# Optimization experiments

Measured on AMD Instinct MI355X. Metric: run time of the kernel, lower is better.

## Reference

```python
import jax, jax.numpy as jnp
import numpy as np

D_IN = 1024
D_OUT = 1024
NUM_HEADS = 16
HEAD_DIM = D_OUT // NUM_HEADS


def setup_inputs() -> dict:
    key = jax.random.key(0)
    ks = jax.random.split(key, 6)
    s = 0.02
    return {
        "x": jax.random.normal(ks[0], (4, 2048, D_IN), dtype=jnp.float32),
        "W_q": jax.random.normal(ks[1], (D_IN, D_OUT), dtype=jnp.float32) * s,
        "W_k": jax.random.normal(ks[2], (D_IN, D_OUT), dtype=jnp.float32) * s,
        "W_v": jax.random.normal(ks[3], (D_IN, D_OUT), dtype=jnp.float32) * s,
        "W_o": jax.random.normal(ks[4], (D_OUT, D_OUT), dtype=jnp.float32) * s,
        "b_o": jax.random.normal(ks[5], (D_OUT,), dtype=jnp.float32) * s,
    }


def reference(x, W_q, W_k, W_v, W_o, b_o):
    b, n, _ = x.shape
    # project and split heads: [b, h, n, d]
    q = (x @ W_q).reshape(b, n, NUM_HEADS, HEAD_DIM).transpose(0, 2, 1, 3)
    k = (x @ W_k).reshape(b, n, NUM_HEADS, HEAD_DIM).transpose(0, 2, 1, 3)
    v = (x @ W_v).reshape(b, n, NUM_HEADS, HEAD_DIM).transpose(0, 2, 1, 3)
    scores = jnp.einsum("bhqd,bhkd->bhqk", q, k)
    causal = jnp.tril(jnp.ones((n, n), dtype=bool))  # True = keep
    scores = jnp.where(causal, scores, -jnp.inf)
    attn = jax.nn.softmax(scores / np.sqrt(HEAD_DIM).astype(np.float32), axis=-1)
    ctx = jnp.einsum("bhqk,bhkd->bhqd", attn, v)
    ctx = ctx.transpose(0, 2, 1, 3).reshape(b, n, D_OUT)
    return ctx @ W_o + b_o
```

## Files before the change

kernel.cpp:

```cpp
#include <hip/hip_runtime.h>
#include <hip/hip_bf16.h>

#define NHEADS 16
#define HDIM 64
#define SEQ 2048
#define BATCH 4
#define DMODEL 1024
#define MTOT (BATCH * SEQ)

typedef short v8s __attribute__((ext_vector_type(8)));
typedef short v4s __attribute__((ext_vector_type(4)));
typedef float v4f __attribute__((ext_vector_type(4)));
typedef unsigned short u16;
typedef unsigned int u32;

__device__ __forceinline__ u16 f2bf(float f) {
    union { float f; unsigned u; } v; v.f = f;
    unsigned r = v.u + 0x7FFFu + ((v.u >> 16) & 1u);
    return (u16)(r >> 16);
}
__device__ __forceinline__ u16 f2bf_fast(float f) {
    union { float f; unsigned u; } v; v.f = f;
    return (u16)((v.u + 0x8000u) >> 16);
}

__device__ __forceinline__ void g2l16(const u16* g, short* l) {
    __builtin_amdgcn_global_load_lds(
        (const __attribute__((address_space(1))) u32*)g,
        (__attribute__((address_space(3))) u32*)l, 16, 0, 0);
}

__global__ __launch_bounds__(256)
void xcvt(const float* __restrict__ x, u16* __restrict__ xb)
{
    size_t i = ((size_t)blockIdx.x * 256 + threadIdx.x) * 8;
    v4f a = *(const v4f*)&x[i];
    v4f b = *(const v4f*)&x[i + 4];
    v8s p;
#pragma unroll
    for (int e = 0; e < 4; ++e) p[e] = (short)f2bf(a[e]);
#pragma unroll
    for (int e = 0; e < 4; ++e) p[4 + e] = (short)f2bf(b[e]);
    *(v8s*)&xb[i] = p;
}

__device__ __forceinline__ void transpose_body(
    const float* __restrict__ src, u16* __restrict__ dst, int k0, int n0)
{
    __shared__ __align__(8) short Ts[64 * 68];
    const int t = threadIdx.x;
    const int n4 = (t & 15) * 4, kl = t >> 4;
#pragma unroll
    for (int it = 0; it < 4; ++it) {
        int k = kl + 16 * it;
        v4f v = *(const v4f*)&src[(size_t)(k0 + k) * DMODEL + n0 + n4];
        v4s p;
#pragma unroll
        for (int e = 0; e < 4; ++e) p[e] = (short)f2bf(v[e]);
        *(v4s*)&Ts[k * 68 + n4] = p;
    }
    __syncthreads();
    const int nl = t >> 4, k4 = (t & 15) * 4;
#pragma unroll
    for (int it = 0; it < 4; ++it) {
        int n = nl + 16 * it;
        v4s o;
#pragma unroll
        for (int e = 0; e < 4; ++e) o[e] = Ts[(k4 + e) * 68 + n];
        *(v4s*)&dst[(size_t)(n0 + n) * DMODEL + k0 + k4] = o;
    }
}

__global__ __launch_bounds__(256)
void transpose_w(const float* __restrict__ src, u16* __restrict__ dst)
{
    transpose_body(src, dst, blockIdx.x * 64, blockIdx.y * 64);
}

__global__ __launch_bounds__(256)
void transpose_w4(const float* __restrict__ s0, const float* __restrict__ s1,
                  const float* __restrict__ s2, const float* __restrict__ s3,
                  u16* __restrict__ dst)
{
    const int z = blockIdx.z;
    const float* src = (z == 0) ? s0 : (z == 1) ? s1 : (z == 2) ? s2 : s3;
    transpose_body(src, dst + (size_t)z * DMODEL * DMODEL,
                   blockIdx.x * 64, blockIdx.y * 64);
}

#define QSCALE (0.125f * 1.44269504088896f)

__device__ __forceinline__ void qkv_epilogue(
    v4f (&acc)[4][4], int which, int n0, int m0, int wn, int wm,
    int l15, int quad, u16* Qb, u16* Kb, u16* Vt)
{
    if (which == 2) {
#pragma unroll
        for (int i = 0; i < 4; ++i)
#pragma unroll
            for (int j = 0; j < 4; ++j) {
                int col = n0 + wn + j * 16 + l15;
                int h = col >> 6, d = col & 63;
                int m = m0 + wm + i * 16 + quad * 4;
                int b = m >> 11, n = m & (SEQ - 1);
                v4s pv;
#pragma unroll
                for (int r = 0; r < 4; ++r) pv[r] = (short)f2bf(acc[i][j][r]);
                *(v4s*)&Vt[((size_t)(b * NHEADS + h) * HDIM + d) * SEQ + n] = pv;
            }
    } else {
        u16* Ob = (which == 0) ? Qb : Kb;
        const float scale = (which == 0) ? QSCALE : 1.0f;
#pragma unroll
        for (int i = 0; i < 4; ++i)
#pragma unroll
            for (int j = 0; j < 4; ++j) {
                int col = n0 + wn + j * 16 + l15;
                int h = col >> 6, d = col & 63;
#pragma unroll
                for (int r = 0; r < 4; ++r) {
                    int m = m0 + wm + i * 16 + quad * 4 + r;
                    int b = m >> 11, n = m & (SEQ - 1);
                    Ob[((size_t)(b * NHEADS + h) * SEQ + n) * HDIM + d] =
                        f2bf(acc[i][j][r] * scale);
                }
            }
    }
}

__global__ __launch_bounds__(256, 2)
void qkv_fast(const u16* __restrict__ xb, const u16* __restrict__ Wt,
              u16* __restrict__ Qb, u16* __restrict__ Kb, u16* __restrict__ Vt)
{
    __shared__ __align__(16) short As[128 * 64];
    __shared__ __align__(16) short Bs[128 * 64];

    const int which = blockIdx.z;
    const u16* W = Wt + (size_t)which * DMODEL * DMODEL;

    const int n0 = blockIdx.x * 128;
    const int m0 = blockIdx.y * 128;
    const int t = threadIdx.x;
    const int lane = t & 63;
    const int l15 = lane & 15;
    const int quad = lane >> 4;
    const int wave = t >> 6;
    const int wm = (wave >> 1) * 64;
    const int wn = (wave & 1) * 64;
    const int srow = t >> 3;
    const int sc8 = (t & 7) * 8;

    v4f acc[4][4];
#pragma unroll
    for (int i = 0; i < 4; ++i)
#pragma unroll
        for (int j = 0; j < 4; ++j) acc[i][j] = {0.f, 0.f, 0.f, 0.f};

    for (int k0 = 0; k0 < DMODEL; k0 += 64) {
        __syncthreads();
#pragma unroll
        for (int c = 0; c < 4; ++c) {
            g2l16(&xb[(size_t)(m0 + c * 32 + srow) * DMODEL + k0 + sc8],
                  &As[(c * 32 + srow) * 64 + sc8]);
            g2l16(&W[(size_t)(n0 + c * 32 + srow) * DMODEL + k0 + sc8],
                  &Bs[(c * 32 + srow) * 64 + sc8]);
        }
        __syncthreads();

#pragma unroll
        for (int kh = 0; kh < 2; ++kh) {
            v8s af[4], bf[4];
#pragma unroll
            for (int i = 0; i < 4; ++i)
                af[i] = *(const v8s*)
                    &As[(wm + i * 16 + l15) * 64 + kh * 32 + quad * 8];
#pragma unroll
            for (int j = 0; j < 4; ++j)
                bf[j] = *(const v8s*)
                    &Bs[(wn + j * 16 + l15) * 64 + kh * 32 + quad * 8];
#pragma unroll
            for (int i = 0; i < 4; ++i)
#pragma unroll
                for (int j = 0; j < 4; ++j)
                    acc[i][j] = __builtin_amdgcn_mfma_f32_16x16x32_bf16(
                        af[i], bf[j], acc[i][j], 0, 0, 0);
        }
    }
    qkv_epilogue(acc, which, n0, m0, wn, wm, l15, quad, Qb, Kb, Vt);
}

__global__ __launch_bounds__(256, 2)
void qkv_slow(const float* __restrict__ x, const u16* __restrict__ Wt,
              u16* __restrict__ Qb, u16* __restrict__ Kb, u16* __restrict__ Vt)
{
    __shared__ __align__(16) short As[128 * 32];
    __shared__ __align__(16) short Bs[128 * 32];

    const int which = blockIdx.z;
    const u16* W = Wt + (size_t)which * DMODEL * DMODEL;

    const int n0 = blockIdx.x * 128;
    const int m0 = blockIdx.y * 128;
    const int t = threadIdx.x;
    const int lane = t & 63;
    const int l15 = lane & 15;
    const int quad = lane >> 4;
    const int wave = t >> 6;
    const int wm = (wave >> 1) * 64;
    const int wn = (wave & 1) * 64;
    const int srow = t >> 2;
    const int sc8 = (t & 3) * 8;

    v4f acc[4][4];
#pragma unroll
    for (int i = 0; i < 4; ++i)
#pragma unroll
        for (int j = 0; j < 4; ++j) acc[i][j] = {0.f, 0.f, 0.f, 0.f};

    for (int k0 = 0; k0 < DMODEL; k0 += 32) {
        __syncthreads();
        g2l16(&W[(size_t)(n0 + srow) * DMODEL + k0 + sc8], &Bs[srow * 32 + sc8]);
        g2l16(&W[(size_t)(n0 + 64 + srow) * DMODEL + k0 + sc8],
              &Bs[(64 + srow) * 32 + sc8]);
#pragma unroll
        for (int it = 0; it < 2; ++it) {
            int row = srow + 64 * it;
            const float* xp = &x[(size_t)(m0 + row) * DMODEL + k0 + sc8];
            v4f x0 = *(const v4f*)xp;
            v4f x1 = *(const v4f*)(xp + 4);
            v8s av;
#pragma unroll
            for (int e = 0; e < 4; ++e) av[e] = (short)f2bf(x0[e]);
#pragma unroll
            for (int e = 0; e < 4; ++e) av[4 + e] = (short)f2bf(x1[e]);
            *(v8s*)&As[row * 32 + sc8] = av;
        }
        __syncthreads();

        v8s af[4], bf[4];
#pragma unroll
        for (int i = 0; i < 4; ++i)
            af[i] = *(const v8s*)&As[(wm + i * 16 + l15) * 32 + quad * 8];
#pragma unroll
        for (int j = 0; j < 4; ++j)
            bf[j] = *(const v8s*)&Bs[(wn + j * 16 + l15) * 32 + quad * 8];
#pragma unroll
        for (int i = 0; i < 4; ++i)
#pragma unroll
            for (int j = 0; j < 4; ++j)
                acc[i][j] = __builtin_amdgcn_mfma_f32_16x16x32_bf16(
                    af[i], bf[j], acc[i][j], 0, 0, 0);
    }
    qkv_epilogue(acc, which, n0, m0, wn, wm, l15, quad, Qb, Kb, Vt);
}

#define KP 72
#define PP 88

__global__ __launch_bounds__(256, 4)
void attn(const u16* __restrict__ Qb, const u16* __restrict__ Kb,
          const u16* __restrict__ Vt, u16* __restrict__ Cx)
{
    __shared__ __align__(16) short Ks[64 * KP];
    __shared__ __align__(16) short Vs[64 * KP];
    __shared__ __align__(16) short Ps[4 * 16 * PP];

    const int ell = blockIdx.x;
    const int xcd = ell & 7;
    const int rest = ell >> 3;
    const int p = rest & 15;
    const int bh = ((rest >> 4) << 3) | xcd;

    const int t = threadIdx.x;
    const int lane = t & 63;
    const int l15 = lane & 15;
    const int quad = lane >> 4;
    const int wave = t >> 6;

    const u16* Qh = Qb + (size_t)bh * SEQ * HDIM;
    const u16* Kh = Kb + (size_t)bh * SEQ * HDIM;
    const u16* Vh = Vt + (size_t)bh * HDIM * SEQ;
    short* Pw = &Ps[wave * 16 * PP];

    const int skey = t >> 2;
    const int sd = (t & 3) * 16;
    const int b = bh >> 4, h = bh & 15;

#pragma unroll 1
    for (int phase = 0; phase < 2; ++phase) {
        const int qt = phase ? p : (31 - p);
        const int q0w = qt * 64 + wave * 16;

        v8s qf[2];
#pragma unroll
        for (int hh = 0; hh < 2; ++hh)
            qf[hh] = *(const v8s*)
                &Qh[(size_t)(q0w + l15) * HDIM + hh * 32 + quad * 8];

        v4f o[4];
        float ls[4];
#pragma unroll
        for (int j = 0; j < 4; ++j) o[j] = {0.f, 0.f, 0.f, 0.f};
#pragma unroll
        for (int r = 0; r < 4; ++r) ls[r] = 0.f;

        v8s pk0, pk1, pv0, pv1;
        {
            const u16* Kp = &Kh[(size_t)skey * HDIM + sd];
            pk0 = *(const v8s*)Kp; pk1 = *(const v8s*)(Kp + 8);
            const u16* Vp = &Vh[(size_t)skey * SEQ + sd];
            pv0 = *(const v8s*)Vp; pv1 = *(const v8s*)(Vp + 8);
        }

#pragma unroll 1
        for (int kb = 0; kb <= qt; ++kb) {
            __syncthreads();
            *(v8s*)&Ks[skey * KP + sd] = pk0;
            *(v8s*)&Ks[skey * KP + sd + 8] = pk1;
            *(v8s*)&Vs[skey * KP + sd] = pv0;
            *(v8s*)&Vs[skey * KP + sd + 8] = pv1;
            __syncthreads();

            if (kb < qt) {
                const u16* Kp = &Kh[(size_t)((kb + 1) * 64 + skey) * HDIM + sd];
                pk0 = *(const v8s*)Kp; pk1 = *(const v8s*)(Kp + 8);
                const u16* Vp = &Vh[(size_t)skey * SEQ + (kb + 1) * 64 + sd];
                pv0 = *(const v8s*)Vp; pv1 = *(const v8s*)(Vp + 8);
            }

            if (kb < qt) {
#pragma unroll
                for (int s = 0; s < 4; ++s) {
                    v8s kf0 = *(const v8s*)&Ks[(s * 16 + l15) * KP + quad * 8];
                    v8s kf1 = *(const v8s*)
                        &Ks[(s * 16 + l15) * KP + 32 + quad * 8];
                    v4f a = {0.f, 0.f, 0.f, 0.f};
                    a = __builtin_amdgcn_mfma_f32_16x16x32_bf16(
                        qf[0], kf0, a, 0, 0, 0);
                    a = __builtin_amdgcn_mfma_f32_16x16x32_bf16(
                        qf[1], kf1, a, 0, 0, 0);
#pragma unroll
                    for (int r = 0; r < 4; ++r) {
                        float pe = exp2f(a[r]);
                        ls[r] += pe;
                        Pw[(quad * 4 + r) * PP + s * 16 + l15] =
                            (short)f2bf_fast(pe);
                    }
                }
            } else {
#pragma unroll
                for (int s = 0; s < 4; ++s) {
                    v8s kf0 = *(const v8s*)&Ks[(s * 16 + l15) * KP + quad * 8];
                    v8s kf1 = *(const v8s*)
                        &Ks[(s * 16 + l15) * KP + 32 + quad * 8];
                    v4f a = {0.f, 0.f, 0.f, 0.f};
                    a = __builtin_amdgcn_mfma_f32_16x16x32_bf16(
                        qf[0], kf0, a, 0, 0, 0);
                    a = __builtin_amdgcn_mfma_f32_16x16x32_bf16(
                        qf[1], kf1, a, 0, 0, 0);
                    int key = kb * 64 + s * 16 + l15;
#pragma unroll
                    for (int r = 0; r < 4; ++r) {
                        int qrow = q0w + quad * 4 + r;
                        float pe = (key > qrow) ? 0.f : exp2f(a[r]);
                        ls[r] += pe;
                        Pw[(quad * 4 + r) * PP + s * 16 + l15] =
                            (short)f2bf_fast(pe);
                    }
                }
            }
            __asm__ volatile("s_waitcnt lgkmcnt(0)" ::: "memory");
#pragma unroll
            for (int ks = 0; ks < 2; ++ks) {
                v8s pa = *(const v8s*)&Pw[l15 * PP + ks * 32 + quad * 8];
#pragma unroll
                for (int j = 0; j < 4; ++j) {
                    v8s vf = *(const v8s*)
                        &Vs[(j * 16 + l15) * KP + ks * 32 + quad * 8];
                    o[j] = __builtin_amdgcn_mfma_f32_16x16x32_bf16(
                        pa, vf, o[j], 0, 0, 0);
                }
            }
        }

#pragma unroll
        for (int r = 0; r < 4; ++r) {
            float v = ls[r];
            v += __shfl_xor(v, 1, 64);
            v += __shfl_xor(v, 2, 64);
            v += __shfl_xor(v, 4, 64);
            v += __shfl_xor(v, 8, 64);
            ls[r] = 1.f / v;
        }
#pragma unroll
        for (int j = 0; j < 4; ++j)
#pragma unroll
            for (int r = 0; r < 4; ++r) {
                int qrow = q0w + quad * 4 + r;
                Cx[((size_t)(b * SEQ + qrow)) * DMODEL + h * HDIM + j * 16 + l15]
                    = f2bf(o[j][r] * ls[r]);
            }
    }
}

__global__ __launch_bounds__(256, 2)
void out_gemm(const u16* __restrict__ Cx, const u16* __restrict__ WoT,
              const float* __restrict__ bo, float* __restrict__ Y)
{
    __shared__ __align__(16) short As[128 * 64];
    __shared__ __align__(16) short Bs[128 * 64];

    const int n0 = blockIdx.x * 128;
    const int m0 = blockIdx.y * 128;
    const int t = threadIdx.x;
    const int lane = t & 63;
    const int l15 = lane & 15;
    const int quad = lane >> 4;
    const int wave = t >> 6;
    const int wm = (wave >> 1) * 64;
    const int wn = (wave & 1) * 64;
    const int srow = t >> 3;
    const int sc8 = (t & 7) * 8;

    v4f acc[4][4];
#pragma unroll
    for (int i = 0; i < 4; ++i)
#pragma unroll
        for (int j = 0; j < 4; ++j) acc[i][j] = {0.f, 0.f, 0.f, 0.f};

    for (int k0 = 0; k0 < DMODEL; k0 += 64) {
        __syncthreads();
#pragma unroll
        for (int c = 0; c < 4; ++c) {
            g2l16(&Cx[(size_t)(m0 + c * 32 + srow) * DMODEL + k0 + sc8],
                  &As[(c * 32 + srow) * 64 + sc8]);
            g2l16(&WoT[(size_t)(n0 + c * 32 + srow) * DMODEL + k0 + sc8],
                  &Bs[(c * 32 + srow) * 64 + sc8]);
        }
        __syncthreads();

#pragma unroll
        for (int kh = 0; kh < 2; ++kh) {
            v8s af[4], bf[4];
#pragma unroll
            for (int i = 0; i < 4; ++i)
                af[i] = *(const v8s*)
                    &As[(wm + i * 16 + l15) * 64 + kh * 32 + quad * 8];
#pragma unroll
            for (int j = 0; j < 4; ++j)
                bf[j] = *(const v8s*)
                    &Bs[(wn + j * 16 + l15) * 64 + kh * 32 + quad * 8];
#pragma unroll
            for (int i = 0; i < 4; ++i)
#pragma unroll
                for (int j = 0; j < 4; ++j)
                    acc[i][j] = __builtin_amdgcn_mfma_f32_16x16x32_bf16(
                        af[i], bf[j], acc[i][j], 0, 0, 0);
        }
    }

#pragma unroll
    for (int i = 0; i < 4; ++i)
#pragma unroll
        for (int j = 0; j < 4; ++j) {
            int col = n0 + wn + j * 16 + l15;
            float bias = bo[col];
#pragma unroll
            for (int r = 0; r < 4; ++r) {
                int m = m0 + wm + i * 16 + quad * 4 + r;
                Y[(size_t)m * DMODEL + col] = acc[i][j][r] + bias;
            }
        }
}

extern "C" void kernel_launch(void* const* d_in, const int* in_sizes, int n_in,
                              void* d_out, int out_size, void* d_ws,
                              size_t ws_size, hipStream_t stream)
{
    const float* x  = (const float*)d_in[0];
    const float* Wq = (const float*)d_in[1];
    const float* Wk = (const float*)d_in[2];
    const float* Wv = (const float*)d_in[3];
    const float* Wo = (const float*)d_in[4];
    const float* bo = (const float*)d_in[5];
    float* Y = (float*)d_out;

    const size_t per = (size_t)BATCH * NHEADS * SEQ * HDIM;
    const size_t wsz = (size_t)DMODEL * DMODEL;
    u16* base = (u16*)d_ws;

    if (ws_size >= (size_t)72 * 1024 * 1024) {
        u16* xb  = base;
        u16* Cx  = base;
        u16* Wt4 = base + per;
        u16* Qb  = base + per + 4 * wsz;
        u16* Kb  = Qb + per;
        u16* Vt  = Kb + per;

        xcvt<<<MTOT * DMODEL / (256 * 8), 256, 0, stream>>>(x, xb);
        transpose_w4<<<dim3(16, 16, 4), 256, 0, stream>>>(Wq, Wk, Wv, Wo, Wt4);
        qkv_fast<<<dim3(DMODEL / 128, MTOT / 128, 3), 256, 0, stream>>>(
            xb, Wt4, Qb, Kb, Vt);
        attn<<<1024, 256, 0, stream>>>(Qb, Kb, Vt, Cx);
        out_gemm<<<dim3(DMODEL / 128, MTOT / 128), 256, 0, stream>>>(
            Cx, Wt4 + 3 * wsz, bo, Y);
    } else {
        u16* Wt  = base;
        u16* Cx  = base;
        u16* Qb  = base + per;
        u16* WoT = base + per;
        u16* Kb  = base + 2 * per;
        u16* Vt  = base + 3 * per;

        transpose_w<<<dim3(16, 16), 256, 0, stream>>>(Wq, Wt);
        transpose_w<<<dim3(16, 16), 256, 0, stream>>>(Wk, Wt + wsz);
        transpose_w<<<dim3(16, 16), 256, 0, stream>>>(Wv, Wt + 2 * wsz);
        qkv_slow<<<dim3(DMODEL / 128, MTOT / 128, 3), 256, 0, stream>>>(
            x, Wt, Qb, Kb, Vt);
        attn<<<1024, 256, 0, stream>>>(Qb, Kb, Vt, Cx);
        transpose_w<<<dim3(16, 16), 256, 0, stream>>>(Wo, WoT);
        out_gemm<<<dim3(DMODEL / 128, MTOT / 128), 256, 0, stream>>>(
            Cx, WoT, bo, Y);
    }
}
```

Before: 274.0 us.

## Rewrite attention with 32x32 MFMA tiles and register-resident P via permlane swap

The attention kernel now gives each wave 32 query rows (a 128-row block tile) and uses 32x32x16 bf16 MFMAs, computing S transposed so the probabilities can be packed straight into A-operand registers with v_cvt_pk_bf16 and v_permlane32_swap. This removes the per-wave P staging buffer in LDS, its waitcnt and round trip, and halves K/V LDS reloads per query row. The grid shrinks to 512 blocks with a launch bound of 2 blocks per CU, so register pressure rises and occupancy and load balance across causal tiles may drop.

Result: faster. 266.5 us (-2.7%).

```diff
diff --git a/kernel.cpp b/kernel.cpp
--- a/kernel.cpp
+++ b/kernel.cpp
@@ -11,6 +11,8 @@
 typedef short v8s __attribute__((ext_vector_type(8)));
 typedef short v4s __attribute__((ext_vector_type(4)));
 typedef float v4f __attribute__((ext_vector_type(4)));
+typedef float v16f __attribute__((ext_vector_type(16)));
+typedef unsigned int v4u __attribute__((ext_vector_type(4)));
 typedef unsigned short u16;
 typedef unsigned int u32;
 
@@ -19,15 +21,31 @@
     unsigned r = v.u + 0x7FFFu + ((v.u >> 16) & 1u);
     return (u16)(r >> 16);
 }
-__device__ __forceinline__ u16 f2bf_fast(float f) {
-    union { float f; unsigned u; } v; v.f = f;
-    return (u16)((v.u + 0x8000u) >> 16);
-}
 
 __device__ __forceinline__ void g2l16(const u16* g, short* l) {
     __builtin_amdgcn_global_load_lds(
         (const __attribute__((address_space(1))) u32*)g,
         (__attribute__((address_space(3))) u32*)l, 16, 0, 0);
+}
+
+__device__ __forceinline__ unsigned pk_bf16(float a, float b) {
+    unsigned r;
+    asm("v_cvt_pk_bf16_f32 %0, %1, %2" : "=v"(r) : "v"(a), "v"(b));
+    return r;
+}
+__device__ __forceinline__ void pl32swap(unsigned& x, unsigned& y) {
+    asm("v_permlane32_swap_b32 %0, %1" : "+v"(x), "+v"(y));
+}
+__device__ __forceinline__ v8s build_pa(float a0, float a1, float a2, float a3,
+                                        float b0, float b1, float b2, float b3) {
+    unsigned X  = pk_bf16(a0, a1);
+    unsigned X2 = pk_bf16(a2, a3);
+    unsigned Y  = pk_bf16(b0, b1);
+    unsigned Y2 = pk_bf16(b2, b3);
+    pl32swap(X, Y);
+    pl32swap(X2, Y2);
+    v4u w; w[0] = X; w[1] = X2; w[2] = Y; w[3] = Y2;
+    return __builtin_bit_cast(v8s, w);
 }
 
 __global__ __launch_bounds__(256)
@@ -255,32 +273,30 @@
 }
 
 #define KP 72
-#define PP 88
-
-__global__ __launch_bounds__(256, 4)
+
+__global__ __launch_bounds__(256, 2)
 void attn(const u16* __restrict__ Qb, const u16* __restrict__ Kb,
           const u16* __restrict__ Vt, u16* __restrict__ Cx)
 {
     __shared__ __align__(16) short Ks[64 * KP];
     __shared__ __align__(16) short Vs[64 * KP];
-    __shared__ __align__(16) short Ps[4 * 16 * PP];
 
     const int ell = blockIdx.x;
     const int xcd = ell & 7;
     const int rest = ell >> 3;
-    const int p = rest & 15;
-    const int bh = ((rest >> 4) << 3) | xcd;
+    const int p = rest & 7;
+    const int bh = ((rest >> 3) << 3) | xcd;
 
     const int t = threadIdx.x;
     const int lane = t & 63;
-    const int l15 = lane & 15;
-    const int quad = lane >> 4;
+    const int l31 = lane & 31;
+    const int hi = lane >> 5;
     const int wave = t >> 6;
+    const int koff = hi * 8;
 
     const u16* Qh = Qb + (size_t)bh * SEQ * HDIM;
     const u16* Kh = Kb + (size_t)bh * SEQ * HDIM;
     const u16* Vh = Vt + (size_t)bh * HDIM * SEQ;
-    short* Pw = &Ps[wave * 16 * PP];
 
     const int skey = t >> 2;
     const int sd = (t & 3) * 16;
@@ -288,118 +304,116 @@
 
 #pragma unroll 1
     for (int phase = 0; phase < 2; ++phase) {
-        const int qt = phase ? p : (31 - p);
-        const int q0w = qt * 64 + wave * 16;
-
-        v8s qf[2];
-#pragma unroll
-        for (int hh = 0; hh < 2; ++hh)
-            qf[hh] = *(const v8s*)
-                &Qh[(size_t)(q0w + l15) * HDIM + hh * 32 + quad * 8];
-
-        v4f o[4];
-        float ls[4];
-#pragma unroll
-        for (int j = 0; j < 4; ++j) o[j] = {0.f, 0.f, 0.f, 0.f};
-#pragma unroll
-        for (int r = 0; r < 4; ++r) ls[r] = 0.f;
-
-        v8s pk0, pk1, pv0, pv1;
+        const int qt = phase ? p : (15 - p);
+        const int q0w = qt * 128 + wave * 32;
+        const int kmax = 2 * qt + 1;
+
+        v8s qf[4];
+#pragma unroll
+        for (int dc = 0; dc < 4; ++dc)
+            qf[dc] = *(const v8s*)
+                &Qh[(size_t)(q0w + l31) * HDIM + dc * 16 + koff];
+
+        v16f o0, o1;
+#pragma unroll
+        for (int r = 0; r < 16; ++r) { o0[r] = 0.f; o1[r] = 0.f; }
+        float ls = 0.f;
+
+        v8s pk0_, pk1_, pv0_, pv1_;
         {
             const u16* Kp = &Kh[(size_t)skey * HDIM + sd];
-            pk0 = *(const v8s*)Kp; pk1 = *(const v8s*)(Kp + 8);
+            pk0_ = *(const v8s*)Kp; pk1_ = *(const v8s*)(Kp + 8);
             const u16* Vp = &Vh[(size_t)skey * SEQ + sd];
-            pv0 = *(const v8s*)Vp; pv1 = *(const v8s*)(Vp + 8);
+            pv0_ = *(const v8s*)Vp; pv1_ = *(const v8s*)(Vp + 8);
         }
 
 #pragma unroll 1
-        for (int kb = 0; kb <= qt; ++kb) {
+        for (int kb = 0; kb <= kmax; ++kb) {
             __syncthreads();
-            *(v8s*)&Ks[skey * KP + sd] = pk0;
-            *(v8s*)&Ks[skey * KP + sd + 8] = pk1;
-            *(v8s*)&Vs[skey * KP + sd] = pv0;
-            *(v8s*)&Vs[skey * KP + sd + 8] = pv1;
+            *(v8s*)&Ks[skey * KP + sd] = pk0_;
+            *(v8s*)&Ks[skey * KP + sd + 8] = pk1_;
+            *(v8s*)&Vs[skey * KP + sd] = pv0_;
+            *(v8s*)&Vs[skey * KP + sd + 8] = pv1_;
             __syncthreads();
 
-            if (kb < qt) {
+            if (kb < kmax) {
                 const u16* Kp = &Kh[(size_t)((kb + 1) * 64 + skey) * HDIM + sd];
-                pk0 = *(const v8s*)Kp; pk1 = *(const v8s*)(Kp + 8);
+                pk0_ = *(const v8s*)Kp; pk1_ = *(const v8s*)(Kp + 8);
                 const u16* Vp = &Vh[(size_t)skey * SEQ + (kb + 1) * 64 + sd];
-                pv0 = *(const v8s*)Vp; pv1 = *(const v8s*)(Vp + 8);
+                pv0_ = *(const v8s*)Vp; pv1_ = *(const v8s*)(Vp + 8);
             }
 
-            if (kb < qt) {
-#pragma unroll
-                for (int s = 0; s < 4; ++s) {
-                    v8s kf0 = *(const v8s*)&Ks[(s * 16 + l15) * KP + quad * 8];
+            if (kb * 64 <= q0w + 31) {
+                const bool diag = (kb * 64 + 63 > q0w);
+                const int qrow = q0w + l31;
+
+                v16f st0, st1;
+#pragma unroll
+                for (int r = 0; r < 16; ++r) { st0[r] = 0.f; st1[r] = 0.f; }
+#pragma unroll
+                for (int dc = 0; dc < 4; ++dc) {
+                    v8s kf0 = *(const v8s*)&Ks[l31 * KP + dc * 16 + koff];
                     v8s kf1 = *(const v8s*)
-                        &Ks[(s * 16 + l15) * KP + 32 + quad * 8];
-                    v4f a = {0.f, 0.f, 0.f, 0.f};
-                    a = __builtin_amdgcn_mfma_f32_16x16x32_bf16(
-                        qf[0], kf0, a, 0, 0, 0);
-                    a = __builtin_amdgcn_mfma_f32_16x16x32_bf16(
-                        qf[1], kf1, a, 0, 0, 0);
-#pragma unroll
-                    for (int r = 0; r < 4; ++r) {
-                        float pe = exp2f(a[r]);
-                        ls[r] += pe;
-                        Pw[(quad * 4 + r) * PP + s * 16 + l15] =
-                            (short)f2bf_fast(pe);
+                        &Ks[(32 + l31) * KP + dc * 16 + koff];
+                    st0 = __builtin_amdgcn_mfma_f32_32x32x16_bf16(
+                        kf0, qf[dc], st0, 0, 0, 0);
+                    st1 = __builtin_amdgcn_mfma_f32_32x32x16_bf16(
+                        kf1, qf[dc], st1, 0, 0, 0);
+                }
+
+                v16f pe0, pe1;
+                if (!diag) {
+#pragma unroll
+                    for (int r = 0; r < 16; ++r) {
+                        pe0[r] = exp2f(st0[r]);
+                        pe1[r] = exp2f(st1[r]);
+                    }
+                } else {
+#pragma unroll
+                    for (int r = 0; r < 16; ++r) {
+                        int kl = kb * 64 + (r & 3) + 8 * (r >> 2) + 4 * hi;
+                        pe0[r] = (kl > qrow) ? 0.f : exp2f(st0[r]);
+                        pe1[r] = (kl + 32 > qrow) ? 0.f : exp2f(st1[r]);
                     }
                 }
-            } else {
-#pragma unroll
-                for (int s = 0; s < 4; ++s) {
-                    v8s kf0 = *(const v8s*)&Ks[(s * 16 + l15) * KP + quad * 8];
-                    v8s kf1 = *(const v8s*)
-                        &Ks[(s * 16 + l15) * KP + 32 + quad * 8];
-                    v4f a = {0.f, 0.f, 0.f, 0.f};
-                    a = __builtin_amdgcn_mfma_f32_16x16x32_bf16(
-                        qf[0], kf0, a, 0, 0, 0);
-                    a = __builtin_amdgcn_mfma_f32_16x16x32_bf16(
-                        qf[1], kf1, a, 0, 0, 0);
-                    int key = kb * 64 + s * 16 + l15;
-#pragma unroll
-                    for (int r = 0; r < 4; ++r) {
-                        int qrow = q0w + quad * 4 + r;
-                        float pe = (key > qrow) ? 0.f : exp2f(a[r]);
-                        ls[r] += pe;
-                        Pw[(quad * 4 + r) * PP + s * 16 + l15] =
-                            (short)f2bf_fast(pe);
-                    }
+#pragma unroll
+                for (int r = 0; r < 16; ++r) ls += pe0[r] + pe1[r];
+
+                v8s pa0 = build_pa(pe0[0], pe0[1], pe0[2], pe0[3],
+                                   pe0[4], pe0[5], pe0[6], pe0[7]);
+                v8s pa1 = build_pa(pe0[8], pe0[9], pe0[10], pe0[11],
+                                   pe0[12], pe0[13], pe0[14], pe0[15]);
+                v8s pa2 = build_pa(pe1[0], pe1[1], pe1[2], pe1[3],
+                                   pe1[4], pe1[5], pe1[6], pe1[7]);
+                v8s pa3 = build_pa(pe1[8], pe1[9], pe1[10], pe1[11],
+                                   pe1[12], pe1[13], pe1[14], pe1[15]);
+
+#pragma unroll
+                for (int kc = 0; kc < 4; ++kc) {
+                    v8s pav = (kc == 0) ? pa0 : (kc == 1) ? pa1
+                              : (kc == 2) ? pa2 : pa3;
+                    v8s vf0 = *(const v8s*)&Vs[l31 * KP + kc * 16 + koff];
+                    v8s vf1 = *(const v8s*)
+                        &Vs[(32 + l31) * KP + kc * 16 + koff];
+                    o0 = __builtin_amdgcn_mfma_f32_32x32x16_bf16(
+                        pav, vf0, o0, 0, 0, 0);
+                    o1 = __builtin_amdgcn_mfma_f32_32x32x16_bf16(
+                        pav, vf1, o1, 0, 0, 0);
                 }
             }
-            __asm__ volatile("s_waitcnt lgkmcnt(0)" ::: "memory");
-#pragma unroll
-            for (int ks = 0; ks < 2; ++ks) {
-                v8s pa = *(const v8s*)&Pw[l15 * PP + ks * 32 + quad * 8];
-#pragma unroll
-                for (int j = 0; j < 4; ++j) {
-                    v8s vf = *(const v8s*)
-                        &Vs[(j * 16 + l15) * KP + ks * 32 + quad * 8];
-                    o[j] = __builtin_amdgcn_mfma_f32_16x16x32_bf16(
-                        pa, vf, o[j], 0, 0, 0);
-                }
-            }
-        }
-
-#pragma unroll
-        for (int r = 0; r < 4; ++r) {
-            float v = ls[r];
-            v += __shfl_xor(v, 1, 64);
-            v += __shfl_xor(v, 2, 64);
-            v += __shfl_xor(v, 4, 64);
-            v += __shfl_xor(v, 8, 64);
-            ls[r] = 1.f / v;
-        }
-#pragma unroll
-        for (int j = 0; j < 4; ++j)
-#pragma unroll
-            for (int r = 0; r < 4; ++r) {
-                int qrow = q0w + quad * 4 + r;
-                Cx[((size_t)(b * SEQ + qrow)) * DMODEL + h * HDIM + j * 16 + l15]
-                    = f2bf(o[j][r] * ls[r]);
-            }
+        }
+
+        ls += __shfl_xor(ls, 32, 64);
+        float inv = 1.f / ls;
+#pragma unroll
+        for (int r = 0; r < 16; ++r) {
+            int m = (r & 3) + 8 * (r >> 2) + 4 * hi;
+            float im = __shfl(inv, m, 64);
+            size_t idx = ((size_t)(b * SEQ + q0w + m)) * DMODEL
+                         + h * HDIM + l31;
+            Cx[idx] = f2bf(o0[r] * im);
+            Cx[idx + 32] = f2bf(o1[r] * im);
+        }
     }
 }
 
@@ -501,7 +515,7 @@
         transpose_w4<<<dim3(16, 16, 4), 256, 0, stream>>>(Wq, Wk, Wv, Wo, Wt4);
         qkv_fast<<<dim3(DMODEL / 128, MTOT / 128, 3), 256, 0, stream>>>(
             xb, Wt4, Qb, Kb, Vt);
-        attn<<<1024, 256, 0, stream>>>(Qb, Kb, Vt, Cx);
+        attn<<<512, 256, 0, stream>>>(Qb, Kb, Vt, Cx);
         out_gemm<<<dim3(DMODEL / 128, MTOT / 128), 256, 0, stream>>>(
             Cx, Wt4 + 3 * wsz, bo, Y);
     } else {
@@ -517,7 +531,7 @@
         transpose_w<<<dim3(16, 16), 256, 0, stream>>>(Wv, Wt + 2 * wsz);
         qkv_slow<<<dim3(DMODEL / 128, MTOT / 128, 3), 256, 0, stream>>>(
             x, Wt, Qb, Kb, Vt);
-        attn<<<1024, 256, 0, stream>>>(Qb, Kb, Vt, Cx);
+        attn<<<512, 256, 0, stream>>>(Qb, Kb, Vt, Cx);
         transpose_w<<<dim3(16, 16), 256, 0, stream>>>(Wo, WoT);
         out_gemm<<<dim3(DMODEL / 128, MTOT / 128), 256, 0, stream>>>(
             Cx, WoT, bo, Y);
```
